# Performance work log

Measured on AMD Instinct MI355X. Metric: run time of the kernel, lower is better.

## Reference

```python
import jax, jax.numpy as jnp
import numpy as np

N = 100000      # total nodes (100 graphs x 1000 nodes each)
G = 100         # graphs per batch
F_IN = 12       # node_features (temporal window)
F_OUT = 32      # DCRNN hidden size (hardcoded in module)
K = 5           # diffusion (Chebyshev) steps (hardcoded)
C = 4           # num_classes
E = 16 * N      # edges: ring (N) + random (15N)


def setup_inputs() -> dict:
    key = jax.random.key(0)
    ks = jax.random.split(key, 12)
    x = jax.random.normal(ks[0], (N, F_IN), dtype=jnp.float32)
    ring = jnp.arange(N, dtype=jnp.int32)
    src = jnp.concatenate([ring, jax.random.randint(ks[1], (15 * N,), 0, N, dtype=jnp.int32)])
    dst = jnp.concatenate([(ring + 1) % N, jax.random.randint(ks[2], (15 * N,), 0, N, dtype=jnp.int32)])
    edge_index = jnp.stack([src, dst])  # [2, E]
    edge_weight = jax.random.uniform(ks[3], (E,), dtype=jnp.float32, minval=0.1, maxval=1.0)
    batch = (jnp.arange(N, dtype=jnp.int32) * G) // N  # sorted graph ids, 1000 nodes per graph
    s = 0.1
    return dict(
        x=x, edge_index=edge_index, edge_weight=edge_weight, batch=batch,
        W_z=jax.random.normal(ks[4], (2, K, F_IN + F_OUT, F_OUT), jnp.float32) * s,
        b_z=jax.random.normal(ks[5], (F_OUT,), jnp.float32) * s,
        W_r=jax.random.normal(ks[6], (2, K, F_IN + F_OUT, F_OUT), jnp.float32) * s,
        b_r=jax.random.normal(ks[7], (F_OUT,), jnp.float32) * s,
        W_h=jax.random.normal(ks[8], (2, K, F_IN + F_OUT, F_OUT), jnp.float32) * s,
        b_h=jax.random.normal(ks[9], (F_OUT,), jnp.float32) * s,
        W_lin=jax.random.normal(ks[10], (F_OUT, C), jnp.float32) * s,
        b_lin=jax.random.normal(ks[11], (C,), jnp.float32) * s,
    )


def reference(x, edge_index, edge_weight, batch, W_z, b_z, W_r, b_r, W_h, b_h, W_lin, b_lin):
    row, col = edge_index[0], edge_index[1]
    # weighted in/out degrees (to_dense_adj sums duplicate edges, same as segment_sum)
    deg_out_inv = 1.0 / jax.ops.segment_sum(edge_weight, row, num_segments=N)
    deg_in_inv = 1.0 / jax.ops.segment_sum(edge_weight, col, num_segments=N)
    norm_out = deg_out_inv[row][:, None]  # per-edge 1/deg_out(src)
    norm_in = deg_in_inv[row][:, None]    # per-edge 1/deg_in(src), as in DConv

    def prop_fwd(h):  # out[dst] += h[src]/deg_out[src]
        return jax.ops.segment_sum(norm_out * h[row], col, num_segments=N)

    def prop_rev(h):  # reverse (transposed) diffusion: out[src] += h[dst]/deg_in[src]
        return jax.ops.segment_sum(norm_in * h[col], row, num_segments=N)

    def dconv(Xc, W, b):
        # Chebyshev diffusion conv, W: [2, K, F_in+F_out, F_out]
        H = Xc @ (W[0, 0] + W[1, 0])
        T1o, T1i = prop_fwd(Xc), prop_rev(Xc)
        H = H + T1o @ W[0, 1] + T1i @ W[1, 1]
        T0o = T0i = Xc
        for k in range(2, K):
            T2o = 2.0 * prop_fwd(T1o) - T0o
            T2i = 2.0 * prop_rev(T1i) - T0i
            H = H + T2o @ W[0, k] + T2i @ W[1, k]
            T0o, T1o = T1o, T2o
            T0i, T1i = T1i, T2i
        return H + b

    # GRU gating with zero-initialized hidden state (H=None in module)
    Hst = jnp.zeros((N, F_OUT), x.dtype)
    XH = jnp.concatenate([x, Hst], axis=1)
    Z = jax.nn.sigmoid(dconv(XH, W_z, b_z))
    R = jax.nn.sigmoid(dconv(XH, W_r, b_r))
    XRH = jnp.concatenate([x, R * Hst], axis=1)
    H_tilde = jnp.tanh(dconv(XRH, W_h, b_h))
    H = Z * Hst + (1.0 - Z) * H_tilde

    h = jax.nn.relu(H) @ W_lin + b_lin            # [N, C]
    sums = jax.ops.segment_sum(h, batch, num_segments=G)
    counts = jax.ops.segment_sum(jnp.ones((N,), h.dtype), batch, num_segments=G)
    return sums / counts[:, None]                 # global_mean_pool -> [G, C]
```

## Files before the change

kernel.cpp:

```cpp
#include <hip/hip_runtime.h>
#include <math.h>

#define NN    100000
#define GG    100
#define FIN   12
#define FOUT  32
#define KD    5
#define CC    4
#define EE    1600000
#define ROWS  108
#define NBF   782
#define NBINS 1564
#define NBC   512
#define CHUNK 3125
#define TOTR  (2 * CHUNK)
#define NSEG  (NBINS * NBC)

__device__ __forceinline__ unsigned bfr(float f) {
    unsigned u = __float_as_uint(f);
    return (u + 0x7FFFu + ((u >> 16) & 1u)) >> 16;
}
__device__ __forceinline__ unsigned pack2(float a, float b) {
    return bfr(a) | (bfr(b) << 16);
}
#define BLO(u) __uint_as_float((u) << 16)
#define BHI(u) __uint_as_float((u) & 0xFFFF0000u)

__device__ __forceinline__ int chunk_of_block(int b) {
    return ((b & 7) << 6) | (b >> 3);
}


__global__ __launch_bounds__(512) void k_hist(const int* __restrict__ ei,
                                              int* __restrict__ hist_g) {
    __shared__ int hist[NBINS];
    for (int i = threadIdx.x; i < NBINS; i += 512) hist[i] = 0;
    __syncthreads();
    int chunk = chunk_of_block(blockIdx.x);
    int lo = chunk * CHUNK, hi = lo + CHUNK;
    for (int e = lo + threadIdx.x; e < hi; e += 512) {
        int s = ei[e], d = ei[EE + e];
        atomicAdd(&hist[d >> 7], 1);
        atomicAdd(&hist[NBF + (s >> 7)], 1);
    }
    __syncthreads();
    for (int i = threadIdx.x; i < NBINS; i += 512)
        hist_g[i * NBC + chunk] = hist[i];
}

__global__ __launch_bounds__(1024) void k_scan1(int* __restrict__ g,
                                                int* __restrict__ bsum) {
    __shared__ int sh[1024];
    int t = threadIdx.x;
    int i = blockIdx.x * 1024 + t;
    int v = g[i];
    sh[t] = v;
    __syncthreads();
    for (int d = 1; d < 1024; d <<= 1) {
        int x = sh[t];
        if (t >= d) x += sh[t - d];
        __syncthreads();
        sh[t] = x;
        __syncthreads();
    }
    g[i] = sh[t] - v;
    if (t == 1023) bsum[blockIdx.x] = sh[1023];
}

__global__ __launch_bounds__(1024) void k_scan2(int* __restrict__ bsum, int nb) {
    __shared__ int sh[1024];
    int t = threadIdx.x;
    int a = (2 * t     < nb) ? bsum[2 * t]     : 0;
    int b = (2 * t + 1 < nb) ? bsum[2 * t + 1] : 0;
    int s = a + b;
    sh[t] = s;
    __syncthreads();
    for (int d = 1; d < 1024; d <<= 1) {
        int x = sh[t];
        if (t >= d) x += sh[t - d];
        __syncthreads();
        sh[t] = x;
        __syncthreads();
    }
    int base = sh[t] - s;
    if (2 * t < nb)     bsum[2 * t] = base;
    if (2 * t + 1 < nb) bsum[2 * t + 1] = base + a;
}

__global__ __launch_bounds__(1024) void k_scan3(int* __restrict__ g,
                                                const int* __restrict__ bsum,
                                                int* __restrict__ off,
                                                int* __restrict__ off_node) {
    int i = blockIdx.x * 1024 + threadIdx.x;
    int v = g[i] + bsum[blockIdx.x];
    g[i] = v;
    if ((i & (NBC - 1)) == 0) off[i / NBC] = v;
    if (i == 0) { off[NBINS] = 2 * EE; off_node[2 * NN] = 2 * EE; }
}

__global__ __launch_bounds__(512) void k_place(const int* __restrict__ ei,
                                               const float* __restrict__ ew,
                                               const int* __restrict__ base_g,
                                               int2* __restrict__ recA) {
    __shared__ int2 ldsrec[TOTR];
    __shared__ int  lofs[NBINS];
    __shared__ int  cur[NBINS];
    __shared__ int  sbase[NBINS];
    __shared__ unsigned short binof[TOTR];
    int* psum = (int*)binof;
    int t = threadIdx.x;
    int chunk = chunk_of_block(blockIdx.x);

    for (int bin = t; bin < NBINS; bin += 512) {
        int b0 = base_g[bin * NBC + chunk];
        int b1;
        if (chunk < NBC - 1)      b1 = base_g[bin * NBC + chunk + 1];
        else if (bin < NBINS - 1) b1 = base_g[(bin + 1) * NBC];
        else                      b1 = 2 * EE;
        sbase[bin] = b0;
        lofs[bin] = b1 - b0;
        cur[bin] = 0;
    }
    __syncthreads();

    int i0 = t * 4;
    int v0 = 0, v1 = 0, v2 = 0, v3 = 0;
    if (i0 + 0 < NBINS) v0 = lofs[i0];
    if (i0 + 1 < NBINS) v1 = lofs[i0 + 1];
    if (i0 + 2 < NBINS) v2 = lofs[i0 + 2];
    if (i0 + 3 < NBINS) v3 = lofs[i0 + 3];
    int s = v0 + v1 + v2 + v3;
    psum[t] = s;
    __syncthreads();
    for (int d = 1; d < 512; d <<= 1) {
        int x = psum[t];
        if (t >= d) x += psum[t - d];
        __syncthreads();
        psum[t] = x;
        __syncthreads();
    }
    int run = psum[t] - s;
    __syncthreads();
    if (i0 + 0 < NBINS) { lofs[i0]     = run; run += v0; }
    if (i0 + 1 < NBINS) { lofs[i0 + 1] = run; run += v1; }
    if (i0 + 2 < NBINS) { lofs[i0 + 2] = run; run += v2; }
    if (i0 + 3 < NBINS) { lofs[i0 + 3] = run; run += v3; }
    __syncthreads();

    int lo = chunk * CHUNK;
    for (int e = lo + t; e < lo + CHUNK; e += 512) {
        int s2 = ei[e], d2 = ei[EE + e];
        float w = ew[e];
        int bf = d2 >> 7;
        int pf = lofs[bf] + atomicAdd(&cur[bf], 1);
        ldsrec[pf] = make_int2(s2 | ((d2 & 127) << 17), __float_as_int(w));
        binof[pf] = (unsigned short)bf;
        int br = NBF + (s2 >> 7);
        int pr = lofs[br] + atomicAdd(&cur[br], 1);
        ldsrec[pr] = make_int2(d2 | ((s2 & 127) << 17), __float_as_int(w));
        binof[pr] = (unsigned short)br;
    }
    __syncthreads();

    for (int i = t; i < TOTR; i += 512) {
        int b = binof[i];
        recA[sbase[b] + (i - lofs[b])] = ldsrec[i];
    }
}

__global__ __launch_bounds__(256) void k_subcsr(
        const int* __restrict__ off, const int2* __restrict__ recA,
        const float* __restrict__ x,
        int* __restrict__ off_node, int* __restrict__ rec2,
        float* __restrict__ dinv_in, float* __restrict__ dinv_out,
        uint2* __restrict__ gA) {
    __shared__ int   hist[128];
    __shared__ int   lofs[128];
    __shared__ int   cur[128];
    __shared__ float wsum[128];
    __shared__ float dl[128];
    int b = blockIdx.x;
    int t = threadIdx.x;
    if (t < 128) { hist[t] = 0; wsum[t] = 0.f; }
    __syncthreads();
    int e0 = off[b], e1 = off[b + 1];
    for (int e = e0 + t; e < e1; e += 256) {
        int2 r = recA[e];
        int loc = r.x >> 17;
        atomicAdd(&hist[loc], 1);
        atomicAdd(&wsum[loc], __int_as_float(r.y));
    }
    __syncthreads();
    if (t < 128) lofs[t] = hist[t];
    __syncthreads();
    for (int d = 1; d < 128; d <<= 1) {
        int v = 0;
        if (t < 128 && t >= d) v = lofs[t - d];
        __syncthreads();
        if (t < 128) lofs[t] += v;
        __syncthreads();
    }
    bool rev = b >= NBF;
    int base = (rev ? b - NBF : b) * 128;
    if (t < 128) {
        int ex = lofs[t] - hist[t];
        lofs[t] = ex;
        cur[t] = 0;
        int node = base + t;
        if (node < NN) {
            off_node[(rev ? NN : 0) + node] = e0 + ex;
            float inv = 1.f / wsum[t];
            dl[t] = inv;
            if (rev) dinv_out[node] = inv;
            else     dinv_in[node]  = inv;
        }
    }
    __syncthreads();
    for (int e = e0 + t; e < e1; e += 256) {
        int rx = recA[e].x;
        int loc = rx >> 17;
        int pos = e0 + lofs[loc] + atomicAdd(&cur[loc], 1);
        rec2[pos] = rx & 0x1FFFF;
    }
    if (rev) {
        __syncthreads();
        for (int i = t; i < 128 * 3; i += 256) {
            int loc = i / 3, cc = i - loc * 3;
            int node = base + loc;
            if (node < NN) {
                float4 v = *(const float4*)(x + (size_t)node * FIN + cc * 4);
                float sc = dl[loc];
                gA[(size_t)node * 3 + cc] =
                    make_uint2(pack2(v.x * sc, v.y * sc), pack2(v.z * sc, v.w * sc));
            }
        }
    }
}


__global__ void k_misc(const float* __restrict__ Wz_in, const float* __restrict__ Wh_in,
                       float* __restrict__ Wz, float* __restrict__ Wh,
                       const float* __restrict__ b_lin, float* __restrict__ out,
                       const float* __restrict__ x, uint2* __restrict__ xb) {
    int t = blockIdx.x * 256 + threadIdx.x;
    if (t < 2 * ROWS * FOUT) {
        int sel = t / (ROWS * FOUT);
        int rem = t - sel * ROWS * FOUT;
        int r = rem / FOUT;
        int f = rem - r * FOUT;
        int b = r / 12;
        int i = r - b * 12;
        const float* Ws = sel ? Wh_in : Wz_in;
        float v;
        if (b == 0)
            v = Ws[(0 * KD + 0) * 44 * 32 + i * 32 + f] + Ws[(1 * KD + 0) * 44 * 32 + i * 32 + f];
        else if (b <= 4)
            v = Ws[(0 * KD + b) * 44 * 32 + i * 32 + f];
        else
            v = Ws[(1 * KD + (b - 4)) * 44 * 32 + i * 32 + f];
        (sel ? Wh : Wz)[r * FOUT + f] = v;
    }
    int u = t - 2 * ROWS * FOUT;
    if (u >= 0 && u < GG * CC) out[u] = b_lin[u & 3];
    if (t < 3 * NN) {
        int n = t / 3, c = t - n * 3;
        float4 v = *(const float4*)(x + (size_t)n * FIN + c * 4);
        xb[(size_t)n * 3 + c] = make_uint2(pack2(v.x, v.y), pack2(v.z, v.w));
    }
}

#define LREC 2048
__global__ __launch_bounds__(256) void k_gather(
        const int* __restrict__ off_node, const int* __restrict__ rec2,
        const uint2* __restrict__ gIn, const uint2* __restrict__ hIn,
        const uint2* __restrict__ prevF, const uint2* __restrict__ prevR,
        const float* __restrict__ dinv_in, const float* __restrict__ dinv_out,
        uint2* __restrict__ outF, uint2* __restrict__ outR,
        uint2* __restrict__ gOut, float c) {
    __shared__ int lrec[LREC];
    int xcd = blockIdx.x & 7;
    int grp = blockIdx.x >> 3;
    bool rev = xcd >= 4;
    int dbase = rev ? NN : 0;
    int ub = (grp * 4 + (xcd & 3)) * 256;
    int lin = ub + threadIdx.x;

    int u1 = ub + 255; if (u1 > 3 * NN - 1) u1 = 3 * NN - 1;
    int node0 = ub / 3, node1 = u1 / 3;
    int w0 = off_node[dbase + node0];
    int w1 = off_node[dbase + node1 + 1];
    int wn = w1 - w0;
    bool useLds = (wn <= LREC);
    if (useLds) {
        for (int i = threadIdx.x; i < wn; i += 256) lrec[i] = rec2[w0 + i];
    }
    __syncthreads();

    if (lin < 3 * NN) {
        int node = lin / 3;
        int ch = lin - node * 3;
        int i0 = dbase + node;
        int e0 = off_node[i0], e1 = off_node[i0 + 1];
        const uint2* in = rev ? hIn : gIn;

        float ax = 0.f, ay = 0.f, az = 0.f, aw = 0.f;
        float bx = 0.f, by = 0.f, bz = 0.f, bw = 0.f;
        if (useLds) {
            int a0 = e0 - w0, a1 = e1 - w0;
            int e = a0;
            for (; e + 7 < a1; e += 8) {
                int n0 = lrec[e],     n1 = lrec[e + 1], n2 = lrec[e + 2], n3 = lrec[e + 3];
                int n4 = lrec[e + 4], n5 = lrec[e + 5], n6 = lrec[e + 6], n7 = lrec[e + 7];
                uint2 v0 = in[(size_t)n0 * 3 + ch];
                uint2 v1 = in[(size_t)n1 * 3 + ch];
                uint2 v2 = in[(size_t)n2 * 3 + ch];
                uint2 v3 = in[(size_t)n3 * 3 + ch];
                uint2 v4 = in[(size_t)n4 * 3 + ch];
                uint2 v5 = in[(size_t)n5 * 3 + ch];
                uint2 v6 = in[(size_t)n6 * 3 + ch];
                uint2 v7 = in[(size_t)n7 * 3 + ch];
                ax += BLO(v0.x); ay += BHI(v0.x); az += BLO(v0.y); aw += BHI(v0.y);
                bx += BLO(v1.x); by += BHI(v1.x); bz += BLO(v1.y); bw += BHI(v1.y);
                ax += BLO(v2.x); ay += BHI(v2.x); az += BLO(v2.y); aw += BHI(v2.y);
                bx += BLO(v3.x); by += BHI(v3.x); bz += BLO(v3.y); bw += BHI(v3.y);
                ax += BLO(v4.x); ay += BHI(v4.x); az += BLO(v4.y); aw += BHI(v4.y);
                bx += BLO(v5.x); by += BHI(v5.x); bz += BLO(v5.y); bw += BHI(v5.y);
                ax += BLO(v6.x); ay += BHI(v6.x); az += BLO(v6.y); aw += BHI(v6.y);
                bx += BLO(v7.x); by += BHI(v7.x); bz += BLO(v7.y); bw += BHI(v7.y);
            }
            for (; e < a1; ++e) {
                int n0 = lrec[e];
                uint2 v0 = in[(size_t)n0 * 3 + ch];
                ax += BLO(v0.x); ay += BHI(v0.x); az += BLO(v0.y); aw += BHI(v0.y);
            }
        } else {
            for (int e = e0; e < e1; ++e) {
                int n0 = rec2[e];
                uint2 v0 = in[(size_t)n0 * 3 + ch];
                ax += BLO(v0.x); ay += BHI(v0.x); az += BLO(v0.y); aw += BHI(v0.y);
            }
        }
        ax += bx; ay += by; az += bz; aw += bw;

        float sc = rev ? c * dinv_in[node] : c;
        ax *= sc; ay *= sc; az *= sc; aw *= sc;

        size_t o = (size_t)node * 3 + ch;
        if (prevF) {
            uint2 p = (rev ? prevR : prevF)[o];
            ax -= BLO(p.x); ay -= BHI(p.x); az -= BLO(p.y); aw -= BHI(p.y);
        }
        (rev ? outR : outF)[o] = make_uint2(pack2(ax, ay), pack2(az, aw));
        if (!rev && gOut) {
            float g = dinv_out[node];
            gOut[o] = make_uint2(pack2(g * ax, g * ay), pack2(g * az, g * aw));
        }
    }
}


__global__ __launch_bounds__(256) void k_fused(
        const float* __restrict__ x, const uint2* __restrict__ TS2,
        const float* __restrict__ Wz, const float* __restrict__ Wh,
        const float* __restrict__ bz, const float* __restrict__ bh,
        const float* __restrict__ Wlin, float* __restrict__ out) {
    __shared__ float rows[128][13];
    __shared__ float red[256 * CC];
    int g = blockIdx.x >> 3;
    int seg = blockIdx.x & 7;
    int base = g * 1000 + seg * 125;
    int tid = threadIdx.x;
    int lane = tid & 63;
    int wave = tid >> 6;
    int f0 = __builtin_amdgcn_readfirstlane(wave * 8);

    float az0[8], ah0[8], az1[8], ah1[8];
#pragma unroll
    for (int fi = 0; fi < 8; ++fi) {
        float vz = bz[f0 + fi], vh = bh[f0 + fi];
        az0[fi] = vz; ah0[fi] = vh; az1[fi] = vz; ah1[fi] = vh;
    }
    bool act1 = (lane + 64) < 125;

    for (int b = 0; b < 9; ++b) {
        __syncthreads();
        if (b == 0) {
            const float* src = x + (size_t)base * FIN;
            for (int q = tid; q < 375; q += 256) {
                float4 v = *(const float4*)(src + q * 4);
                int e = q * 4;
                int n0 = e / 12,       i0 = e - n0 * 12;       rows[n0][i0] = v.x;
                int n1 = (e + 1) / 12, i1 = (e + 1) - n1 * 12; rows[n1][i1] = v.y;
                int n2 = (e + 2) / 12, i2 = (e + 2) - n2 * 12; rows[n2][i2] = v.z;
                int n3 = (e + 3) / 12, i3 = (e + 3) - n3 * 12; rows[n3][i3] = v.w;
            }
        } else {
            const uint2* Tb = TS2 + (size_t)(b - 1) * NN * 3;
            for (int q = tid; q < 375; q += 256) {
                int n = q / 3, cc = q - n * 3;
                uint2 v = Tb[(size_t)(base + n) * 3 + cc];
                rows[n][cc * 4 + 0] = BLO(v.x);
                rows[n][cc * 4 + 1] = BHI(v.x);
                rows[n][cc * 4 + 2] = BLO(v.y);
                rows[n][cc * 4 + 3] = BHI(v.y);
            }
        }
        __syncthreads();
        const float* wzr = Wz + b * 12 * FOUT + f0;
        const float* whr = Wh + b * 12 * FOUT + f0;
#pragma unroll
        for (int i = 0; i < FIN; ++i) {
            float v0 = rows[lane][i];
            float v1 = rows[lane + 64][i];
#pragma unroll
            for (int fi = 0; fi < 8; ++fi) {
                float wz = wzr[i * FOUT + fi];
                float wh = whr[i * FOUT + fi];
                az0[fi] = fmaf(v0, wz, az0[fi]);
                az1[fi] = fmaf(v1, wz, az1[fi]);
                ah0[fi] = fmaf(v0, wh, ah0[fi]);
                ah1[fi] = fmaf(v1, wh, ah1[fi]);
            }
        }
    }

    float o[CC] = {0.f, 0.f, 0.f, 0.f};
#pragma unroll
    for (int fi = 0; fi < 8; ++fi) {
        float z = 1.f / (1.f + __expf(-az0[fi]));
        float e2 = __expf(2.f * ah0[fi]);
        float th = 1.f - 2.f / (e2 + 1.f);
        float hv = fmaxf((1.f - z) * th, 0.f);
#pragma unroll
        for (int c = 0; c < CC; ++c) o[c] = fmaf(hv, Wlin[(f0 + fi) * 4 + c], o[c]);
    }
    if (act1) {
#pragma unroll
        for (int fi = 0; fi < 8; ++fi) {
            float z = 1.f / (1.f + __expf(-az1[fi]));
            float e2 = __expf(2.f * ah1[fi]);
            float th = 1.f - 2.f / (e2 + 1.f);
            float hv = fmaxf((1.f - z) * th, 0.f);
#pragma unroll
            for (int c = 0; c < CC; ++c) o[c] = fmaf(hv, Wlin[(f0 + fi) * 4 + c], o[c]);
        }
    }

#pragma unroll
    for (int c = 0; c < CC; ++c) red[tid * CC + c] = o[c];
    __syncthreads();
    for (int st = 128; st > 0; st >>= 1) {
        if (tid < st) {
#pragma unroll
            for (int c = 0; c < CC; ++c) red[tid * CC + c] += red[(tid + st) * CC + c];
        }
        __syncthreads();
    }
    if (tid == 0) {
#pragma unroll
        for (int c = 0; c < CC; ++c) atomicAdd(out + g * CC + c, red[c] * 0.001f);
    }
}


extern "C" void kernel_launch(void* const* d_in, const int* in_sizes, int n_in,
                              void* d_out, int out_size, void* d_ws, size_t ws_size,
                              hipStream_t stream) {
    const float* x     = (const float*)d_in[0];
    const int*   ei    = (const int*)d_in[1];
    const float* ew    = (const float*)d_in[2];
    const float* W_z   = (const float*)d_in[4];
    const float* b_z   = (const float*)d_in[5];
    const float* W_h   = (const float*)d_in[8];
    const float* b_h   = (const float*)d_in[9];
    const float* W_lin = (const float*)d_in[10];
    const float* b_lin = (const float*)d_in[11];
    float* out = (float*)d_out;

    int*   rec2     = (int*)d_ws;
    unsigned* TSb   = (unsigned*)(rec2 + 2 * (size_t)EE);
    int2*  recA     = (int2*)TSb;
    int*   hist_g   = rec2;
    int*   bsumS    = rec2 + NSEG;
    unsigned* gAu   = TSb + (size_t)8 * NN * 6 + 1600000;
    unsigned* gBu   = gAu + (size_t)NN * 6;
    unsigned* xbu   = gBu + (size_t)NN * 6;
    float* dinv_in  = (float*)(xbu + (size_t)NN * 6);
    float* dinv_out = dinv_in + NN;
    float* Wz       = dinv_out + NN;
    float* Wh       = Wz + ROWS * FOUT;
    int*   off      = (int*)(Wh + ROWS * FOUT);
    int*   off_node = off + NBINS + 1;

    uint2* TS2 = (uint2*)TSb;
    uint2* T1o = TS2 + (size_t)0 * NN * 3;
    uint2* T2o = TS2 + (size_t)1 * NN * 3;
    uint2* T3o = TS2 + (size_t)2 * NN * 3;
    uint2* T4o = TS2 + (size_t)3 * NN * 3;
    uint2* T1i = TS2 + (size_t)4 * NN * 3;
    uint2* T2i = TS2 + (size_t)5 * NN * 3;
    uint2* T3i = TS2 + (size_t)6 * NN * 3;
    uint2* T4i = TS2 + (size_t)7 * NN * 3;
    uint2* gA = (uint2*)gAu;
    uint2* gB = (uint2*)gBu;
    uint2* xb = (uint2*)xbu;

    dim3 B(256);
    int nbG = 2344;
    int nbScan = NSEG / 1024;
    int nbMisc = (3 * NN + 255) / 256;

    k_hist<<<NBC, 512, 0, stream>>>(ei, hist_g);
    k_scan1<<<nbScan, 1024, 0, stream>>>(hist_g, bsumS);
    k_scan2<<<1, 1024, 0, stream>>>(bsumS, nbScan);
    k_scan3<<<nbScan, 1024, 0, stream>>>(hist_g, bsumS, off, off_node);
    k_place<<<NBC, 512, 0, stream>>>(ei, ew, hist_g, recA);
    k_subcsr<<<NBINS, B, 0, stream>>>(off, recA, x, off_node, rec2, dinv_in, dinv_out, gA);

    k_misc<<<nbMisc, B, 0, stream>>>(W_z, W_h, Wz, Wh, b_lin, out, x, xb);

    k_gather<<<nbG, B, 0, stream>>>(off_node, rec2, gA, xb,  nullptr, nullptr, dinv_in, dinv_out, T1o, T1i, gB, 1.f);
    k_gather<<<nbG, B, 0, stream>>>(off_node, rec2, gB, T1i, xb,      xb,      dinv_in, dinv_out, T2o, T2i, gA, 2.f);
    k_gather<<<nbG, B, 0, stream>>>(off_node, rec2, gA, T2i, T1o,     T1i,     dinv_in, dinv_out, T3o, T3i, gB, 2.f);
    k_gather<<<nbG, B, 0, stream>>>(off_node, rec2, gB, T3i, T2o,     T2i,     dinv_in, dinv_out, T4o, T4i, nullptr, 2.f);

    k_fused<<<8 * GG, B, 0, stream>>>(x, TS2, Wz, Wh, b_z, b_h, W_lin, out);
}
```

Baseline: 290.2 us.

## Fold misc prep into scan1, drop scan2, stage subCSR records in LDS

The weight repacking, output bias init and bf16 conversion of x move from a separate kernel into k_scan1. The single-block k_scan2 is removed; each k_scan3 block now reduces the preceding block sums itself in shared memory. k_subcsr caches its bin's records in LDS (up to 3072) so the second pass reads LDS instead of re-reading global memory. The aim is two fewer launches and less global traffic, at the cost of redundant block-sum reductions and extra LDS use that may lower occupancy.

```diff
diff --git a/kernel.cpp b/kernel.cpp
--- a/kernel.cpp
+++ b/kernel.cpp
@@ -15,6 +15,7 @@
 #define CHUNK 3125
 #define TOTR  (2 * CHUNK)
 #define NSEG  (NBINS * NBC)
+#define SUBMAX 3072
 
 __device__ __forceinline__ unsigned bfr(float f) {
     unsigned u = __float_as_uint(f);
@@ -48,8 +49,12 @@
         hist_g[i * NBC + chunk] = hist[i];
 }
 
-__global__ __launch_bounds__(1024) void k_scan1(int* __restrict__ g,
-                                                int* __restrict__ bsum) {
+__global__ __launch_bounds__(1024) void k_scan1(
+        int* __restrict__ g, int* __restrict__ bsum,
+        const float* __restrict__ Wz_in, const float* __restrict__ Wh_in,
+        float* __restrict__ Wz, float* __restrict__ Wh,
+        const float* __restrict__ b_lin, float* __restrict__ out,
+        const float* __restrict__ x, uint2* __restrict__ xb) {
     __shared__ int sh[1024];
     int t = threadIdx.x;
     int i = blockIdx.x * 1024 + t;
@@ -57,42 +62,56 @@
     sh[t] = v;
     __syncthreads();
     for (int d = 1; d < 1024; d <<= 1) {
-        int x = sh[t];
-        if (t >= d) x += sh[t - d];
-        __syncthreads();
-        sh[t] = x;
+        int x2 = sh[t];
+        if (t >= d) x2 += sh[t - d];
+        __syncthreads();
+        sh[t] = x2;
         __syncthreads();
     }
     g[i] = sh[t] - v;
     if (t == 1023) bsum[blockIdx.x] = sh[1023];
-}
-
-__global__ __launch_bounds__(1024) void k_scan2(int* __restrict__ bsum, int nb) {
-    __shared__ int sh[1024];
-    int t = threadIdx.x;
-    int a = (2 * t     < nb) ? bsum[2 * t]     : 0;
-    int b = (2 * t + 1 < nb) ? bsum[2 * t + 1] : 0;
-    int s = a + b;
-    sh[t] = s;
-    __syncthreads();
-    for (int d = 1; d < 1024; d <<= 1) {
-        int x = sh[t];
-        if (t >= d) x += sh[t - d];
-        __syncthreads();
-        sh[t] = x;
-        __syncthreads();
-    }
-    int base = sh[t] - s;
-    if (2 * t < nb)     bsum[2 * t] = base;
-    if (2 * t + 1 < nb) bsum[2 * t + 1] = base + a;
+
+    if (i < 2 * ROWS * FOUT) {
+        int sel = i / (ROWS * FOUT);
+        int rem = i - sel * ROWS * FOUT;
+        int r = rem / FOUT;
+        int f = rem - r * FOUT;
+        int b = r / 12;
+        int ii = r - b * 12;
+        const float* Ws = sel ? Wh_in : Wz_in;
+        float vv;
+        if (b == 0)
+            vv = Ws[(0 * KD + 0) * 44 * 32 + ii * 32 + f] + Ws[(1 * KD + 0) * 44 * 32 + ii * 32 + f];
+        else if (b <= 4)
+            vv = Ws[(0 * KD + b) * 44 * 32 + ii * 32 + f];
+        else
+            vv = Ws[(1 * KD + (b - 4)) * 44 * 32 + ii * 32 + f];
+        (sel ? Wh : Wz)[r * FOUT + f] = vv;
+    }
+    int u = i - 2 * ROWS * FOUT;
+    if (u >= 0 && u < GG * CC) out[u] = b_lin[u & 3];
+    if (i < 3 * NN) {
+        int n = i / 3, c = i - n * 3;
+        float4 vf = *(const float4*)(x + (size_t)n * FIN + c * 4);
+        xb[(size_t)n * 3 + c] = make_uint2(pack2(vf.x, vf.y), pack2(vf.z, vf.w));
+    }
 }
 
 __global__ __launch_bounds__(1024) void k_scan3(int* __restrict__ g,
                                                 const int* __restrict__ bsum,
                                                 int* __restrict__ off,
                                                 int* __restrict__ off_node) {
-    int i = blockIdx.x * 1024 + threadIdx.x;
-    int v = g[i] + bsum[blockIdx.x];
+    __shared__ int sh[1024];
+    int t = threadIdx.x;
+    sh[t] = (t < blockIdx.x) ? bsum[t] : 0;
+    __syncthreads();
+    for (int d = 512; d > 0; d >>= 1) {
+        if (t < d) sh[t] += sh[t + d];
+        __syncthreads();
+    }
+    int base = sh[0];
+    int i = blockIdx.x * 1024 + t;
+    int v = g[i] + base;
     g[i] = v;
     if ((i & (NBC - 1)) == 0) off[i / NBC] = v;
     if (i == 0) { off[NBINS] = 2 * EE; off_node[2 * NN] = 2 * EE; }
@@ -174,6 +193,7 @@
         int* __restrict__ off_node, int* __restrict__ rec2,
         float* __restrict__ dinv_in, float* __restrict__ dinv_out,
         uint2* __restrict__ gA) {
+    __shared__ int2  seg[SUBMAX];
     __shared__ int   hist[128];
     __shared__ int   lofs[128];
     __shared__ int   cur[128];
@@ -184,11 +204,23 @@
     if (t < 128) { hist[t] = 0; wsum[t] = 0.f; }
     __syncthreads();
     int e0 = off[b], e1 = off[b + 1];
-    for (int e = e0 + t; e < e1; e += 256) {
-        int2 r = recA[e];
-        int loc = r.x >> 17;
-        atomicAdd(&hist[loc], 1);
-        atomicAdd(&wsum[loc], __int_as_float(r.y));
+    int cnt = e1 - e0;
+    bool stg = (cnt <= SUBMAX);
+    if (stg) {
+        for (int i = t; i < cnt; i += 256) {
+            int2 r = recA[e0 + i];
+            seg[i] = r;
+            int loc = r.x >> 17;
+            atomicAdd(&hist[loc], 1);
+            atomicAdd(&wsum[loc], __int_as_float(r.y));
+        }
+    } else {
+        for (int i = t; i < cnt; i += 256) {
+            int2 r = recA[e0 + i];
+            int loc = r.x >> 17;
+            atomicAdd(&hist[loc], 1);
+            atomicAdd(&wsum[loc], __int_as_float(r.y));
+        }
     }
     __syncthreads();
     if (t < 128) lofs[t] = hist[t];
@@ -216,11 +248,20 @@
         }
     }
     __syncthreads();
-    for (int e = e0 + t; e < e1; e += 256) {
-        int rx = recA[e].x;
-        int loc = rx >> 17;
-        int pos = e0 + lofs[loc] + atomicAdd(&cur[loc], 1);
-        rec2[pos] = rx & 0x1FFFF;
+    if (stg) {
+        for (int i = t; i < cnt; i += 256) {
+            int rx = seg[i].x;
+            int loc = rx >> 17;
+            int pos = e0 + lofs[loc] + atomicAdd(&cur[loc], 1);
+            rec2[pos] = rx & 0x1FFFF;
+        }
+    } else {
+        for (int i = t; i < cnt; i += 256) {
+            int rx = recA[e0 + i].x;
+            int loc = rx >> 17;
+            int pos = e0 + lofs[loc] + atomicAdd(&cur[loc], 1);
+            rec2[pos] = rx & 0x1FFFF;
+        }
     }
     if (rev) {
         __syncthreads();
@@ -234,38 +275,6 @@
                     make_uint2(pack2(v.x * sc, v.y * sc), pack2(v.z * sc, v.w * sc));
             }
         }
-    }
-}
-
-
-__global__ void k_misc(const float* __restrict__ Wz_in, const float* __restrict__ Wh_in,
-                       float* __restrict__ Wz, float* __restrict__ Wh,
-                       const float* __restrict__ b_lin, float* __restrict__ out,
-                       const float* __restrict__ x, uint2* __restrict__ xb) {
-    int t = blockIdx.x * 256 + threadIdx.x;
-    if (t < 2 * ROWS * FOUT) {
-        int sel = t / (ROWS * FOUT);
-        int rem = t - sel * ROWS * FOUT;
-        int r = rem / FOUT;
-        int f = rem - r * FOUT;
-        int b = r / 12;
-        int i = r - b * 12;
-        const float* Ws = sel ? Wh_in : Wz_in;
-        float v;
-        if (b == 0)
-            v = Ws[(0 * KD + 0) * 44 * 32 + i * 32 + f] + Ws[(1 * KD + 0) * 44 * 32 + i * 32 + f];
-        else if (b <= 4)
-            v = Ws[(0 * KD + b) * 44 * 32 + i * 32 + f];
-        else
-            v = Ws[(1 * KD + (b - 4)) * 44 * 32 + i * 32 + f];
-        (sel ? Wh : Wz)[r * FOUT + f] = v;
-    }
-    int u = t - 2 * ROWS * FOUT;
-    if (u >= 0 && u < GG * CC) out[u] = b_lin[u & 3];
-    if (t < 3 * NN) {
-        int n = t / 3, c = t - n * 3;
-        float4 v = *(const float4*)(x + (size_t)n * FIN + c * 4);
-        xb[(size_t)n * 3 + c] = make_uint2(pack2(v.x, v.y), pack2(v.z, v.w));
     }
 }
 
@@ -508,16 +517,12 @@
     dim3 B(256);
     int nbG = 2344;
     int nbScan = NSEG / 1024;
-    int nbMisc = (3 * NN + 255) / 256;
 
     k_hist<<<NBC, 512, 0, stream>>>(ei, hist_g);
-    k_scan1<<<nbScan, 1024, 0, stream>>>(hist_g, bsumS);
-    k_scan2<<<1, 1024, 0, stream>>>(bsumS, nbScan);
+    k_scan1<<<nbScan, 1024, 0, stream>>>(hist_g, bsumS, W_z, W_h, Wz, Wh, b_lin, out, x, xb);
     k_scan3<<<nbScan, 1024, 0, stream>>>(hist_g, bsumS, off, off_node);
     k_place<<<NBC, 512, 0, stream>>>(ei, ew, hist_g, recA);
     k_subcsr<<<NBINS, B, 0, stream>>>(off, recA, x, off_node, rec2, dinv_in, dinv_out, gA);
-
-    k_misc<<<nbMisc, B, 0, stream>>>(W_z, W_h, Wz, Wh, b_lin, out, x, xb);
 
     k_gather<<<nbG, B, 0, stream>>>(off_node, rec2, gA, xb,  nullptr, nullptr, dinv_in, dinv_out, T1o, T1i, gB, 1.f);
     k_gather<<<nbG, B, 0, stream>>>(off_node, rec2, gB, T1i, xb,      xb,      dinv_in, dinv_out, T2o, T2i, gA, 2.f);
```

Result: no change. 285.4 us (median of 3 runs) (-1.7%).
